# Performance work log

Measured on AMD Instinct MI355X. Metric: run time of the kernel, lower is better.

The kernel has to match this reference:

```python
import jax, jax.numpy as jnp
import numpy as np

B, T, C = 2, 2048, 2048
N_HEAD, N_KV_HEAD = 16, 4
HEAD_DIM = C // N_HEAD  # 128
EPS = 1e-6


def rms_norm(x):
    # no learned scale, normalize over head_dim (last axis)
    return x * jax.lax.rsqrt(jnp.mean(jnp.square(x), axis=-1, keepdims=True) + EPS)


def apply_rotary_emb(x, cos, sin):
    # x: [B, T, H, D]; cos/sin: [T, D/2]  (rotate-half RoPE)
    x1, x2 = jnp.split(x, 2, axis=-1)
    c = cos[None, :, None, :]
    s = sin[None, :, None, :]
    return jnp.concatenate([x1 * c - x2 * s, x1 * s + x2 * c], axis=-1)


def setup_inputs() -> dict:
    key = jax.random.key(0)
    ks = jax.random.split(key, 6)
    x = jax.random.normal(ks[0], (B, T, C), dtype=jnp.float32)
    # real rotary tables: theta = 10000^{-2i/D}
    inv_freq = 1.0 / (10000.0 ** (jnp.arange(0, HEAD_DIM, 2, dtype=jnp.float32) / HEAD_DIM))
    angles = jnp.arange(T, dtype=jnp.float32)[:, None] * inv_freq[None, :]  # [T, D/2]
    cos, sin = jnp.cos(angles), jnp.sin(angles)
    std = 0.02
    Wq = jax.random.normal(ks[1], (C, N_HEAD * HEAD_DIM), dtype=jnp.float32) * std
    Wk = jax.random.normal(ks[2], (C, N_KV_HEAD * HEAD_DIM), dtype=jnp.float32) * std
    Wv = jax.random.normal(ks[3], (C, N_KV_HEAD * HEAD_DIM), dtype=jnp.float32) * std
    Wp = jax.random.normal(ks[4], (C, C), dtype=jnp.float32) * std
    return {"x": x, "cos": cos, "sin": sin, "Wq": Wq, "Wk": Wk, "Wv": Wv, "Wp": Wp}


def reference(x, cos, sin, Wq, Wk, Wv, Wp):
    Bx, Tx, Cx = x.shape
    q = (x @ Wq).reshape(Bx, Tx, N_HEAD, HEAD_DIM)
    k = (x @ Wk).reshape(Bx, Tx, N_KV_HEAD, HEAD_DIM)
    v = (x @ Wv).reshape(Bx, Tx, N_KV_HEAD, HEAD_DIM)
    q = rms_norm(apply_rotary_emb(q, cos, sin))
    k = rms_norm(apply_rotary_emb(k, cos, sin))
    # module scales q by 1/sqrt(D) AND nn.dot_product_attention scales again
    q = q * (1.0 / jnp.sqrt(HEAD_DIM))
    # GQA head repeat
    n_rep = N_HEAD // N_KV_HEAD
    k = jnp.repeat(k, n_rep, axis=2)  # [B, T, H, D]
    v = jnp.repeat(v, n_rep, axis=2)
    scores = jnp.einsum("bthd,bshd->bhts", q, k) / jnp.sqrt(jnp.asarray(HEAD_DIM, x.dtype))
    causal = jnp.tril(jnp.ones((Tx, Tx), dtype=bool))  # key <= query
    scores = jnp.where(causal[None, None, :, :], scores, jnp.finfo(scores.dtype).min)
    probs = jax.nn.softmax(scores, axis=-1)
    y = jnp.einsum("bhts,bshd->bthd", probs, v).reshape(Bx, Tx, Cx)
    return y @ Wp
```

## Files before the change

kernel.cpp:

```cpp
#include <hip/hip_runtime.h>
#include <hip/hip_bf16.h>
#include <math.h>

#define B_  2
#define T_  2048
#define C_  2048
#define NH_ 16
#define NKV_ 4
#define HD_ 128
#define NREP_ (NH_/NKV_)

#define QKVLD 3072
#define KOFF  2048
#define VOFF  2560

#define QSCALE 0.01127105500694502f

typedef __bf16 bf16x8 __attribute__((ext_vector_type(8)));
typedef float  f32x4  __attribute__((ext_vector_type(4)));
typedef float  f32x16 __attribute__((ext_vector_type(16)));

__device__ inline void gload_lds16(const void* g, void* l) {
    __builtin_amdgcn_global_load_lds((const __attribute__((address_space(1))) void*)g,
                                     (__attribute__((address_space(3))) void*)l, 16, 0, 0);
}

__global__ __launch_bounds__(256) void cast_bf16(const float* __restrict__ src,
                                                 __bf16* __restrict__ dst)
{
    size_t i = ((size_t)blockIdx.x * 256 + threadIdx.x) * 8;
    float4 a = *(const float4*)&src[i];
    float4 b = *(const float4*)&src[i + 4];
    union { __bf16 h[8]; uint4 u; } pk;
    pk.h[0] = (__bf16)a.x; pk.h[1] = (__bf16)a.y; pk.h[2] = (__bf16)a.z; pk.h[3] = (__bf16)a.w;
    pk.h[4] = (__bf16)b.x; pk.h[5] = (__bf16)b.y; pk.h[6] = (__bf16)b.z; pk.h[7] = (__bf16)b.w;
    *(uint4*)&dst[i] = pk.u;
}

__global__ __launch_bounds__(256) void wtrans_qkv(const float* __restrict__ Wq,
                                                  const float* __restrict__ Wk,
                                                  const float* __restrict__ Wv,
                                                  __bf16* __restrict__ dst)
{
    __shared__ float tl[32][33];
    int ct = blockIdx.x;
    int k0 = blockIdx.y * 32;
    const float* src;
    int ncols, c0, dr0;
    if (ct < 64)      { src = Wq; ncols = 2048; c0 = ct * 32;        dr0 = ct * 32; }
    else if (ct < 80) { src = Wk; ncols = 512;  c0 = (ct - 64) * 32; dr0 = KOFF + (ct - 64) * 32; }
    else              { src = Wv; ncols = 512;  c0 = (ct - 80) * 32; dr0 = VOFF + (ct - 80) * 32; }

    int tid = threadIdx.x;
    int r  = tid >> 3;
    int c4 = (tid & 7) * 4;
    float4 v = *(const float4*)&src[(size_t)(k0 + r) * ncols + c0 + c4];
    tl[r][c4] = v.x; tl[r][c4 + 1] = v.y; tl[r][c4 + 2] = v.z; tl[r][c4 + 3] = v.w;
    __syncthreads();
    union { __bf16 h[4]; uint2 u; } pk;
#pragma unroll
    for (int j = 0; j < 4; ++j) pk.h[j] = (__bf16)tl[c4 + j][r];
    *(uint2*)&dst[(size_t)(dr0 + r) * 2048 + k0 + c4] = pk.u;
}

__global__ __launch_bounds__(256) void wtrans(const float* __restrict__ src,
                                              __bf16* __restrict__ dst, int ncols)
{
    __shared__ float tl[32][33];
    int n0 = blockIdx.x * 32;
    int k0 = blockIdx.y * 32;
    int tid = threadIdx.x;
    int r  = tid >> 3;
    int c4 = (tid & 7) * 4;
    float4 v = *(const float4*)&src[(size_t)(k0 + r) * ncols + n0 + c4];
    tl[r][c4] = v.x; tl[r][c4 + 1] = v.y; tl[r][c4 + 2] = v.z; tl[r][c4 + 3] = v.w;
    __syncthreads();
    union { __bf16 h[4]; uint2 u; } pk;
#pragma unroll
    for (int j = 0; j < 4; ++j) pk.h[j] = (__bf16)tl[c4 + j][r];
    *(uint2*)&dst[(size_t)(n0 + r) * 2048 + k0 + c4] = pk.u;
}

template<typename TOUT>
__global__ __launch_bounds__(256) void gemm_bt(const __bf16* __restrict__ A,
                                               const __bf16* __restrict__ Bt,
                                               TOUT* __restrict__ C,
                                               int M, int N, int K, int ldc)
{
    __shared__ __bf16 As[2][128 * 32];
    __shared__ __bf16 Bs[2][128 * 32];

    const int tid  = threadIdx.x;
    const int wv   = tid >> 6;
    const int lane = tid & 63;
    const int grp  = lane >> 4;
    const int id16 = lane & 15;
    const int wr   = wv >> 1;
    const int wc   = wv & 1;

    const int row0 = blockIdx.y * 128;
    const int col0 = blockIdx.x * 128;

    const int sm = tid >> 2;
    const int sk = (tid & 3) << 3;

    const __bf16* ga0 = A  + (size_t)(row0 + sm) * K + sk;
    const __bf16* ga1 = A  + (size_t)(row0 + 64 + sm) * K + sk;
    const __bf16* gb0 = Bt + (size_t)(col0 + sm) * K + sk;
    const __bf16* gb1 = Bt + (size_t)(col0 + 64 + sm) * K + sk;

    f32x4 acc[4][4];
    const f32x4 fz = {0.f, 0.f, 0.f, 0.f};
#pragma unroll
    for (int i = 0; i < 4; ++i)
#pragma unroll
        for (int j = 0; j < 4; ++j) acc[i][j] = fz;

    const int nk = K >> 5;

    {
        __bf16* a0 = &As[0][wv << 9];
        __bf16* b0 = &Bs[0][wv << 9];
        gload_lds16(ga0, a0);
        gload_lds16(ga1, a0 + 2048);
        gload_lds16(gb0, b0);
        gload_lds16(gb1, b0 + 2048);
    }

    for (int kt = 0; kt < nk; ++kt) {
        const int bufc = kt & 1;
        asm volatile("s_waitcnt vmcnt(0)" ::: "memory");
        __syncthreads();

        if (kt + 1 < nk) {
            const int kb = (kt + 1) << 5;
            __bf16* a0 = &As[1 - bufc][wv << 9];
            __bf16* b0 = &Bs[1 - bufc][wv << 9];
            gload_lds16(ga0 + kb, a0);
            gload_lds16(ga1 + kb, a0 + 2048);
            gload_lds16(gb0 + kb, b0);
            gload_lds16(gb1 + kb, b0 + 2048);
        }

        bf16x8 af[4], bfr[4];
#pragma unroll
        for (int i = 0; i < 4; ++i)
            af[i] = *(const bf16x8*)&As[bufc][((wr << 6) + (i << 4) + id16) * 32 + (grp << 3)];
#pragma unroll
        for (int j = 0; j < 4; ++j)
            bfr[j] = *(const bf16x8*)&Bs[bufc][((wc << 6) + (j << 4) + id16) * 32 + (grp << 3)];
#pragma unroll
        for (int i = 0; i < 4; ++i)
#pragma unroll
            for (int j = 0; j < 4; ++j)
                acc[i][j] = __builtin_amdgcn_mfma_f32_16x16x32_bf16(af[i], bfr[j], acc[i][j], 0, 0, 0);
    }

#pragma unroll
    for (int i = 0; i < 4; ++i) {
        int gr = row0 + (wr << 6) + (i << 4) + (grp << 2);
#pragma unroll
        for (int j = 0; j < 4; ++j) {
            int gc = col0 + (wc << 6) + (j << 4) + id16;
#pragma unroll
            for (int r = 0; r < 4; ++r) {
                if constexpr (sizeof(TOUT) == 4)
                    C[(size_t)(gr + r) * ldc + gc] = acc[i][j][r];
                else
                    C[(size_t)(gr + r) * ldc + gc] = (TOUT)acc[i][j][r];
            }
        }
    }
}

__global__ __launch_bounds__(256) void rope_rms_b(__bf16* __restrict__ base,
                                                  const float* __restrict__ cosb,
                                                  const float* __restrict__ sinb,
                                                  int nheads, float scale)
{
    int wid  = blockIdx.x * 4 + (threadIdx.x >> 6);
    int lane = threadIdx.x & 63;
    int bt = wid / nheads;
    int hd = wid % nheads;
    int t  = bt % T_;

    __bf16* p = base + (size_t)bt * QKVLD + hd * HD_;
    float c = cosb[t * 64 + lane];
    float s = sinb[t * 64 + lane];
    float x1 = (float)p[lane];
    float x2 = (float)p[lane + 64];
    float r1 = x1 * c - x2 * s;
    float r2 = x1 * s + x2 * c;
    float ss = r1 * r1 + r2 * r2;
#pragma unroll
    for (int off = 32; off; off >>= 1) ss += __shfl_xor(ss, off, 64);
    float inv = rsqrtf(ss * (1.f / 128.f) + 1e-6f) * scale;
    p[lane]      = (__bf16)(r1 * inv);
    p[lane + 64] = (__bf16)(r2 * inv);
}

__global__ __launch_bounds__(256) void vtrans(const __bf16* __restrict__ qkv,
                                              __bf16* __restrict__ vt)
{
    __shared__ __bf16 tl[32][HD_ + 8];
    int bx  = blockIdx.x;
    int st  = bx & 63;
    int bkv = bx >> 6;
    int b = bkv >> 2, kv = bkv & 3;
    int s0 = st << 5;
    int tid = threadIdx.x;
    {
        int s = tid >> 3;
        int d = (tid & 7) << 4;
        const __bf16* src = qkv + (size_t)(b * T_ + s0 + s) * QKVLD + VOFF + kv * HD_ + d;
        *(bf16x8*)&tl[s][d]     = *(const bf16x8*)src;
        *(bf16x8*)&tl[s][d + 8] = *(const bf16x8*)(src + 8);
    }
    __syncthreads();
    {
        int d  = tid >> 1;
        int sh = (tid & 1) << 4;
        __bf16 tmp[16];
#pragma unroll
        for (int j = 0; j < 16; ++j) tmp[j] = tl[sh + j][d];
        __bf16* dst = vt + ((size_t)(b * NKV_ + kv) * HD_ + d) * T_ + s0 + sh;
        *(bf16x8*)dst       = *(bf16x8*)&tmp[0];
        *(bf16x8*)(dst + 8) = *(bf16x8*)&tmp[8];
    }
}

__global__ __launch_bounds__(256, 2) void attn32(const __bf16* __restrict__ qkv,
                                                 const __bf16* __restrict__ vbT,
                                                 __bf16* __restrict__ y,
                                                 float* __restrict__ pOA,
                                                 float* __restrict__ pOB,
                                                 float* __restrict__ pLA,
                                                 float* __restrict__ pLB)
{
    __shared__ __bf16 Ks[2][64 * 128];
    __shared__ __bf16 Vs[2][64 * 128];

    const int tid  = threadIdx.x;
    const int wv   = tid >> 6;
    const int lane = tid & 63;
    const int l31  = lane & 31;
    const int h32  = lane >> 5;

    const int bx   = blockIdx.x;
    const int b    = (bx >> 2) & 1;
    const int kv   = bx & 3;
    const int m    = bx >> 3;
    const int hh   = m & 3;
    const int role = (m >> 2) & 1;
    const int p    = m >> 3;
    const int h    = kv * 4 + hh;
    const int bh   = b * 16 + h;
    const int slot = p * 32 + bh;

    const int hi  = 15 - p;
    const int lo  = p;
    const int tts = role ? (15 - 2 * p) : 99;

    auto KT = [&](int t) { return role ? (t < tts ? 17 + t : t - tts) : t; };

    int qw0 = hi * 128 + wv * 32;
    int qme = qw0 + l31;

    uint koff[4], voff[4];
#pragma unroll
    for (int i = 0; i < 4; ++i) {
        int r  = (wv * 4 + i) * 4 + (lane >> 4);
        int c  = lane & 15;
        int cs = c ^ (r & 15);
        koff[i] = (uint)(r * (QKVLD * 2) + cs * 16);
        int d   = r + ((cs >> 3) << 6);
        voff[i] = (uint)(d * (T_ * 2) + (cs & 7) * 16);
    }
    const char* kg = (const char*)(qkv + (size_t)b * T_ * QKVLD + KOFF + kv * HD_);
    const char* vg = (const char*)(vbT + ((size_t)(b * NKV_ + kv) * HD_) * T_);

    uint off8[8];
#pragma unroll
    for (int s = 0; s < 8; ++s)
        off8[s] = (uint)(l31 * 256 + ((((s << 1) + h32) ^ (l31 & 15)) << 4));

#define STAGE(BUF, KN)                                                        \
    {                                                                         \
        const char* kp = kg + (size_t)(KN) * (64 * QKVLD * 2);                \
        const char* vp = vg + (size_t)(KN) * (64 * 2);                        \
        __bf16* kl = &Ks[BUF][(wv * 4) * 512];                                \
        __bf16* vl = &Vs[BUF][(wv * 4) * 512];                                \
        _Pragma("unroll")                                                     \
        for (int i = 0; i < 4; ++i) gload_lds16(kp + koff[i], kl + i * 512);  \
        _Pragma("unroll")                                                     \
        for (int i = 0; i < 4; ++i) gload_lds16(vp + voff[i], vl + i * 512);  \
    }

    bf16x8 qf[8], qf2[8];
    {
        const __bf16* qp = qkv + (size_t)(b * T_ + hi * 128 + wv * 32 + l31) * QKVLD + h * HD_ + h32 * 8;
#pragma unroll
        for (int s = 0; s < 8; ++s) qf[s] = *(const bf16x8*)(qp + s * 16);
        const __bf16* qp2 = qkv + (size_t)(b * T_ + lo * 128 + wv * 32 + l31) * QKVLD + h * HD_ + h32 * 8;
#pragma unroll
        for (int s = 0; s < 8; ++s) qf2[s] = *(const bf16x8*)(qp2 + s * 16);
    }

    f32x16 o[4];
#pragma unroll
    for (int dt = 0; dt < 4; ++dt)
#pragma unroll
        for (int r = 0; r < 16; ++r) o[dt][r] = 0.f;
    float l_p = 0.f;

#define STORE_PARTIAL(PO, PL)                                                   \
    {                                                                           \
        float lsum = l_p + __shfl_xor(l_p, 32, 64);                             \
        int qloc = wv * 32 + l31;                                               \
        float* po = (PO) + ((size_t)slot * 128 + qloc) * 128;                   \
        _Pragma("unroll")                                                       \
        for (int dt = 0; dt < 4; ++dt)                                          \
            _Pragma("unroll")                                                   \
            for (int g = 0; g < 4; ++g) {                                       \
                float4 f = {o[dt][4 * g + 0], o[dt][4 * g + 1],                 \
                            o[dt][4 * g + 2], o[dt][4 * g + 3]};                \
                *(float4*)&po[dt * 32 + 8 * g + 4 * h32] = f;                   \
            }                                                                   \
        if (h32 == 0) (PL)[slot * 128 + qloc] = lsum;                           \
    }

#define TILE_BODY(TT, BUFC)                                                     \
    {                                                                           \
        const int tt_ = (TT);                                                   \
        asm volatile("s_waitcnt vmcnt(0)" ::: "memory");                        \
        __syncthreads();                                                        \
        if (tt_ + 1 < 17) { int kn_ = KT(tt_ + 1); STAGE(1 - (BUFC), kn_); }    \
        if (role && tt_ == tts) {                                               \
            STORE_PARTIAL(pOB, pLB);                                            \
            _Pragma("unroll")                                                   \
            for (int dt = 0; dt < 4; ++dt)                                      \
                _Pragma("unroll")                                               \
                for (int r = 0; r < 16; ++r) o[dt][r] = 0.f;                    \
            l_p = 0.f;                                                          \
            _Pragma("unroll")                                                   \
            for (int s = 0; s < 8; ++s) qf[s] = qf2[s];                         \
            qw0 = lo * 128 + wv * 32;                                           \
            qme = qw0 + l31;                                                    \
        }                                                                       \
        const int s0 = KT(tt_) << 6;                                            \
        if (s0 <= qw0 + 31) {                                                   \
            const char* Kb = (const char*)&Ks[BUFC][0];                         \
            const char* Vb = (const char*)&Vs[BUFC][0];                         \
            f32x16 S0, S1;                                                      \
            _Pragma("unroll")                                                   \
            for (int r = 0; r < 16; ++r) { S0[r] = 0.f; S1[r] = 0.f; }          \
            __builtin_amdgcn_s_setprio(1);                                      \
            _Pragma("unroll")                                                   \
            for (int s = 0; s < 8; ++s) {                                       \
                bf16x8 kf0 = *(const bf16x8*)(Kb + off8[s]);                    \
                bf16x8 kf1 = *(const bf16x8*)(Kb + off8[s] + 8192);             \
                S0 = __builtin_amdgcn_mfma_f32_32x32x16_bf16(kf0, qf[s], S0, 0, 0, 0); \
                S1 = __builtin_amdgcn_mfma_f32_32x32x16_bf16(kf1, qf[s], S1, 0, 0, 0); \
            }                                                                   \
            __builtin_amdgcn_s_setprio(0);                                      \
            const bool domask = (s0 + 63 > qw0);                                \
            uint w[16];                                                         \
            _Pragma("unroll")                                                   \
            for (int i = 0; i < 8; ++i) {                                       \
                const int r0 = 2 * i;                                           \
                float e0 = exp2f(S0[r0]);                                       \
                float e1 = exp2f(S0[r0 + 1]);                                   \
                if (domask) {                                                   \
                    int k0 = s0 + (r0 & 3) + 8 * (r0 >> 2) + 4 * h32;           \
                    if (k0     > qme) e0 = 0.f;                                 \
                    if (k0 + 1 > qme) e1 = 0.f;                                 \
                }                                                               \
                l_p += e0 + e1;                                                 \
                union { __bf16 h2[2]; uint u; } pk;                             \
                pk.h2[0] = (__bf16)e0; pk.h2[1] = (__bf16)e1;                   \
                w[i] = pk.u;                                                    \
            }                                                                   \
            _Pragma("unroll")                                                   \
            for (int i = 0; i < 8; ++i) {                                       \
                const int r0 = 2 * i;                                           \
                float e0 = exp2f(S1[r0]);                                       \
                float e1 = exp2f(S1[r0 + 1]);                                   \
                if (domask) {                                                   \
                    int k0 = s0 + 32 + (r0 & 3) + 8 * (r0 >> 2) + 4 * h32;      \
                    if (k0     > qme) e0 = 0.f;                                 \
                    if (k0 + 1 > qme) e1 = 0.f;                                 \
                }                                                               \
                l_p += e0 + e1;                                                 \
                union { __bf16 h2[2]; uint u; } pk;                             \
                pk.h2[0] = (__bf16)e0; pk.h2[1] = (__bf16)e1;                   \
                w[8 + i] = pk.u;                                                \
            }                                                                   \
            union U8 { uint u[4]; bf16x8 v; };                                  \
            bf16x8 pf[4];                                                       \
            _Pragma("unroll")                                                   \
            for (int ks = 0; ks < 4; ++ks) {                                    \
                const int bsel = ((ks >> 1) << 3) + ((ks & 1) << 2);            \
                uint sa = h32 ? w[bsel]     : w[bsel + 2];                      \
                uint sb = h32 ? w[bsel + 1] : w[bsel + 3];                      \
                uint g0 = (uint)__shfl_xor((int)sa, 32, 64);                    \
                uint g1 = (uint)__shfl_xor((int)sb, 32, 64);                    \
                U8 t;                                                           \
                if (h32 == 0) {                                                 \
                    t.u[0] = w[bsel];     t.u[1] = w[bsel + 1];                 \
                    t.u[2] = g0;          t.u[3] = g1;                          \
                } else {                                                        \
                    t.u[0] = g0;          t.u[1] = g1;                          \
                    t.u[2] = w[bsel + 2]; t.u[3] = w[bsel + 3];                 \
                }                                                               \
                pf[ks] = t.v;                                                   \
            }                                                                   \
            __builtin_amdgcn_s_setprio(1);                                      \
            _Pragma("unroll")                                                   \
            for (int dt = 0; dt < 4; ++dt) {                                    \
                const int ab = (dt >> 1) << 2;                                  \
                const int hf = (dt & 1) * 8192;                                 \
                _Pragma("unroll")                                               \
                for (int ks = 0; ks < 4; ++ks) {                                \
                    bf16x8 vf = *(const bf16x8*)(Vb + off8[ab + ks] + hf);      \
                    o[dt] = __builtin_amdgcn_mfma_f32_32x32x16_bf16(vf, pf[ks], o[dt], 0, 0, 0); \
                }                                                               \
            }                                                                   \
            __builtin_amdgcn_s_setprio(0);                                      \
        }                                                                       \
    }

    STAGE(0, KT(0));

    for (int tt = 0; tt < 16; tt += 2) {
        TILE_BODY(tt, 0);
        TILE_BODY(tt + 1, 1);
    }
    TILE_BODY(16, 0);

    if (role == 0) {
        STORE_PARTIAL(pOA, pLA);
    } else {
        float l  = l_p + __shfl_xor(l_p, 32, 64);
        float inv = 1.f / l;
        __bf16* yp = y + (size_t)(b * T_ + qw0 + l31) * C_ + h * HD_;
#pragma unroll
        for (int dt = 0; dt < 4; ++dt)
#pragma unroll
            for (int g = 0; g < 4; ++g) {
                union { __bf16 h4[4]; uint2 u; } pk;
#pragma unroll
                for (int e = 0; e < 4; ++e) pk.h4[e] = (__bf16)(o[dt][4 * g + e] * inv);
                *(uint2*)&yp[dt * 32 + 8 * g + 4 * h32] = pk.u;
            }
    }
#undef TILE_BODY
#undef STORE_PARTIAL
#undef STAGE
}

__global__ __launch_bounds__(256) void attn_combine(const float* __restrict__ pOA,
                                                    const float* __restrict__ pOB,
                                                    const float* __restrict__ pLA,
                                                    const float* __restrict__ pLB,
                                                    __bf16* __restrict__ y)
{
    int slot = blockIdx.x;
    int p  = slot >> 5, bh = slot & 31;
    int b  = bh >> 4,   h  = bh & 15;
    int hi = 15 - p;
    int t  = threadIdx.x;
    int q  = t >> 1;
    int dh = (t & 1) << 6;

    float inv = 1.f / (pLA[slot * 128 + q] + pLB[slot * 128 + q]);
    size_t base = ((size_t)slot * 128 + q) * 128 + dh;
    __bf16* yp = y + (size_t)(b * T_ + hi * 128 + q) * C_ + h * HD_ + dh;
#pragma unroll
    for (int d0 = 0; d0 < 64; d0 += 8) {
        float4 a0 = *(const float4*)&pOA[base + d0];
        float4 a1 = *(const float4*)&pOA[base + d0 + 4];
        float4 b0 = *(const float4*)&pOB[base + d0];
        float4 b1 = *(const float4*)&pOB[base + d0 + 4];
        union { __bf16 h8[8]; uint4 u; } pk;
        pk.h8[0] = (__bf16)((a0.x + b0.x) * inv);
        pk.h8[1] = (__bf16)((a0.y + b0.y) * inv);
        pk.h8[2] = (__bf16)((a0.z + b0.z) * inv);
        pk.h8[3] = (__bf16)((a0.w + b0.w) * inv);
        pk.h8[4] = (__bf16)((a1.x + b1.x) * inv);
        pk.h8[5] = (__bf16)((a1.y + b1.y) * inv);
        pk.h8[6] = (__bf16)((a1.z + b1.z) * inv);
        pk.h8[7] = (__bf16)((a1.w + b1.w) * inv);
        *(uint4*)&yp[d0] = pk.u;
    }
}

extern "C" void kernel_launch(void* const* d_in, const int* in_sizes, int n_in,
                              void* d_out, int out_size, void* d_ws, size_t ws_size,
                              hipStream_t stream)
{
    const float* x    = (const float*)d_in[0];
    const float* cosb = (const float*)d_in[1];
    const float* sinb = (const float*)d_in[2];
    const float* Wq   = (const float*)d_in[3];
    const float* Wk   = (const float*)d_in[4];
    const float* Wv   = (const float*)d_in[5];
    const float* Wp   = (const float*)d_in[6];
    float* out = (float*)d_out;

    const int M = B_ * T_;

    char* w = (char*)d_ws;
    __bf16* xb    = (__bf16*)w;  w += (size_t)M * C_ * 2;
    __bf16* qkv   = (__bf16*)w;  w += (size_t)M * QKVLD * 2;
    __bf16* wqkvT = (__bf16*)w;  w += (size_t)QKVLD * C_ * 2;
    __bf16* wpT   = (__bf16*)w;  w += (size_t)C_ * C_ * 2;
    __bf16* vt    = (__bf16*)w;  w += (size_t)M * NKV_ * HD_ * 2;
    __bf16* y     = (__bf16*)w;  w += (size_t)M * C_ * 2;
    float*  pOB   = (float*)w;
    float*  pOA   = (float*)xb;
    float*  pLA   = (float*)wqkvT;
    float*  pLB   = pLA + 8 * 32 * 128;

    cast_bf16<<<(M * C_) / 2048, 256, 0, stream>>>(x, xb);
    wtrans_qkv<<<dim3(96, C_ / 32), 256, 0, stream>>>(Wq, Wk, Wv, wqkvT);
    wtrans<<<dim3(C_ / 32, C_ / 32), 256, 0, stream>>>(Wp, wpT, C_);

    gemm_bt<__bf16><<<dim3(QKVLD / 128, M / 128), 256, 0, stream>>>(xb, wqkvT, qkv, M, QKVLD, C_, QKVLD);

    rope_rms_b<<<(M * NH_) / 4, 256, 0, stream>>>(qkv, cosb, sinb, NH_, QSCALE);
    rope_rms_b<<<(M * NKV_) / 4, 256, 0, stream>>>(qkv + KOFF, cosb, sinb, NKV_, 1.0f);

    vtrans<<<B_ * NKV_ * (T_ / 32), 256, 0, stream>>>(qkv, vt);

    attn32<<<512, 256, 0, stream>>>(qkv, vt, y, pOA, pOB, pLA, pLB);
    attn_combine<<<256, 256, 0, stream>>>(pOA, pOB, pLA, pLB, y);

    gemm_bt<float><<<dim3(C_ / 128, M / 128), 256, 0, stream>>>(y, wpT, out, M, C_, C_, C_);
}
```

Measured before the change: 326.5 us.

## Merge prep and rope/vtrans launches; fold split-attention combine into attention via tickets

Merges the cast and the two weight-transpose kernels into one prep launch, and the Q and K rope/rms passes plus the V transpose into one launch, which also zeroes the per-slot ticket counters. The separate attn_combine kernel is removed. Each split-attention block now writes its partial, fences, and takes an atomic ticket, and the second block to finish reads the other's partial and writes the normalized output. This removes several launches and one full pass over the partial buffers, at the cost of fences, atomics and an extra block barrier inside the attention kernel.

```diff
diff --git a/kernel.cpp b/kernel.cpp
--- a/kernel.cpp
+++ b/kernel.cpp
@@ -25,60 +25,56 @@
                                      (__attribute__((address_space(3))) void*)l, 16, 0, 0);
 }
 
-__global__ __launch_bounds__(256) void cast_bf16(const float* __restrict__ src,
-                                                 __bf16* __restrict__ dst)
-{
-    size_t i = ((size_t)blockIdx.x * 256 + threadIdx.x) * 8;
-    float4 a = *(const float4*)&src[i];
-    float4 b = *(const float4*)&src[i + 4];
-    union { __bf16 h[8]; uint4 u; } pk;
-    pk.h[0] = (__bf16)a.x; pk.h[1] = (__bf16)a.y; pk.h[2] = (__bf16)a.z; pk.h[3] = (__bf16)a.w;
-    pk.h[4] = (__bf16)b.x; pk.h[5] = (__bf16)b.y; pk.h[6] = (__bf16)b.z; pk.h[7] = (__bf16)b.w;
-    *(uint4*)&dst[i] = pk.u;
-}
-
-__global__ __launch_bounds__(256) void wtrans_qkv(const float* __restrict__ Wq,
-                                                  const float* __restrict__ Wk,
-                                                  const float* __restrict__ Wv,
-                                                  __bf16* __restrict__ dst)
+__global__ __launch_bounds__(256) void prep(const float* __restrict__ x,
+                                            const float* __restrict__ Wq,
+                                            const float* __restrict__ Wk,
+                                            const float* __restrict__ Wv,
+                                            const float* __restrict__ Wp,
+                                            __bf16* __restrict__ xb,
+                                            __bf16* __restrict__ wqkvT,
+                                            __bf16* __restrict__ wpT)
 {
     __shared__ float tl[32][33];
-    int ct = blockIdx.x;
-    int k0 = blockIdx.y * 32;
+    const int bx  = blockIdx.x;
+    const int tid = threadIdx.x;
+
+    if (bx < 4096) {
+        size_t i = ((size_t)bx * 256 + tid) * 8;
+        float4 a = *(const float4*)&x[i];
+        float4 b = *(const float4*)&x[i + 4];
+        union { __bf16 h[8]; uint4 u; } pk;
+        pk.h[0] = (__bf16)a.x; pk.h[1] = (__bf16)a.y; pk.h[2] = (__bf16)a.z; pk.h[3] = (__bf16)a.w;
+        pk.h[4] = (__bf16)b.x; pk.h[5] = (__bf16)b.y; pk.h[6] = (__bf16)b.z; pk.h[7] = (__bf16)b.w;
+        *(uint4*)&xb[i] = pk.u;
+        return;
+    }
+
     const float* src;
-    int ncols, c0, dr0;
-    if (ct < 64)      { src = Wq; ncols = 2048; c0 = ct * 32;        dr0 = ct * 32; }
-    else if (ct < 80) { src = Wk; ncols = 512;  c0 = (ct - 64) * 32; dr0 = KOFF + (ct - 64) * 32; }
-    else              { src = Wv; ncols = 512;  c0 = (ct - 80) * 32; dr0 = VOFF + (ct - 80) * 32; }
-
-    int tid = threadIdx.x;
-    int r  = tid >> 3;
+    int ncols, c0, dr0, k0;
+    if (bx < 10240) {
+        int r  = bx - 4096;
+        int ct = r % 96;
+        k0 = (r / 96) * 32;
+        if (ct < 64)      { src = Wq; ncols = 2048; c0 = ct * 32;        dr0 = ct * 32; }
+        else if (ct < 80) { src = Wk; ncols = 512;  c0 = (ct - 64) * 32; dr0 = KOFF + (ct - 64) * 32; }
+        else              { src = Wv; ncols = 512;  c0 = (ct - 80) * 32; dr0 = VOFF + (ct - 80) * 32; }
+    } else {
+        int r  = bx - 10240;
+        src = Wp; ncols = 2048;
+        c0  = (r & 63) * 32; dr0 = c0;
+        k0  = (r >> 6) * 32;
+    }
+    __bf16* dst = (bx < 10240) ? wqkvT : wpT;
+
+    int rr = tid >> 3;
     int c4 = (tid & 7) * 4;
-    float4 v = *(const float4*)&src[(size_t)(k0 + r) * ncols + c0 + c4];
-    tl[r][c4] = v.x; tl[r][c4 + 1] = v.y; tl[r][c4 + 2] = v.z; tl[r][c4 + 3] = v.w;
+    float4 v = *(const float4*)&src[(size_t)(k0 + rr) * ncols + c0 + c4];
+    tl[rr][c4] = v.x; tl[rr][c4 + 1] = v.y; tl[rr][c4 + 2] = v.z; tl[rr][c4 + 3] = v.w;
     __syncthreads();
     union { __bf16 h[4]; uint2 u; } pk;
 #pragma unroll
-    for (int j = 0; j < 4; ++j) pk.h[j] = (__bf16)tl[c4 + j][r];
-    *(uint2*)&dst[(size_t)(dr0 + r) * 2048 + k0 + c4] = pk.u;
-}
-
-__global__ __launch_bounds__(256) void wtrans(const float* __restrict__ src,
-                                              __bf16* __restrict__ dst, int ncols)
-{
-    __shared__ float tl[32][33];
-    int n0 = blockIdx.x * 32;
-    int k0 = blockIdx.y * 32;
-    int tid = threadIdx.x;
-    int r  = tid >> 3;
-    int c4 = (tid & 7) * 4;
-    float4 v = *(const float4*)&src[(size_t)(k0 + r) * ncols + n0 + c4];
-    tl[r][c4] = v.x; tl[r][c4 + 1] = v.y; tl[r][c4 + 2] = v.z; tl[r][c4 + 3] = v.w;
-    __syncthreads();
-    union { __bf16 h[4]; uint2 u; } pk;
-#pragma unroll
-    for (int j = 0; j < 4; ++j) pk.h[j] = (__bf16)tl[c4 + j][r];
-    *(uint2*)&dst[(size_t)(n0 + r) * 2048 + k0 + c4] = pk.u;
+    for (int j = 0; j < 4; ++j) pk.h[j] = (__bf16)tl[c4 + j][rr];
+    *(uint2*)&dst[(size_t)(dr0 + rr) * 2048 + k0 + c4] = pk.u;
 }
 
 template<typename TOUT>
@@ -173,60 +169,66 @@
     }
 }
 
-__global__ __launch_bounds__(256) void rope_rms_b(__bf16* __restrict__ base,
-                                                  const float* __restrict__ cosb,
-                                                  const float* __restrict__ sinb,
-                                                  int nheads, float scale)
-{
-    int wid  = blockIdx.x * 4 + (threadIdx.x >> 6);
-    int lane = threadIdx.x & 63;
-    int bt = wid / nheads;
-    int hd = wid % nheads;
-    int t  = bt % T_;
-
-    __bf16* p = base + (size_t)bt * QKVLD + hd * HD_;
-    float c = cosb[t * 64 + lane];
-    float s = sinb[t * 64 + lane];
-    float x1 = (float)p[lane];
-    float x2 = (float)p[lane + 64];
-    float r1 = x1 * c - x2 * s;
-    float r2 = x1 * s + x2 * c;
-    float ss = r1 * r1 + r2 * r2;
-#pragma unroll
-    for (int off = 32; off; off >>= 1) ss += __shfl_xor(ss, off, 64);
-    float inv = rsqrtf(ss * (1.f / 128.f) + 1e-6f) * scale;
-    p[lane]      = (__bf16)(r1 * inv);
-    p[lane + 64] = (__bf16)(r2 * inv);
-}
-
-__global__ __launch_bounds__(256) void vtrans(const __bf16* __restrict__ qkv,
-                                              __bf16* __restrict__ vt)
+__global__ __launch_bounds__(256) void rope_vt(__bf16* __restrict__ qkv,
+                                               const float* __restrict__ cosb,
+                                               const float* __restrict__ sinb,
+                                               __bf16* __restrict__ vt,
+                                               int* __restrict__ flags)
 {
     __shared__ __bf16 tl[32][HD_ + 8];
-    int bx  = blockIdx.x;
-    int st  = bx & 63;
-    int bkv = bx >> 6;
-    int b = bkv >> 2, kv = bkv & 3;
-    int s0 = st << 5;
-    int tid = threadIdx.x;
-    {
-        int s = tid >> 3;
-        int d = (tid & 7) << 4;
-        const __bf16* src = qkv + (size_t)(b * T_ + s0 + s) * QKVLD + VOFF + kv * HD_ + d;
-        *(bf16x8*)&tl[s][d]     = *(const bf16x8*)src;
-        *(bf16x8*)&tl[s][d + 8] = *(const bf16x8*)(src + 8);
-    }
-    __syncthreads();
-    {
-        int d  = tid >> 1;
-        int sh = (tid & 1) << 4;
-        __bf16 tmp[16];
-#pragma unroll
-        for (int j = 0; j < 16; ++j) tmp[j] = tl[sh + j][d];
-        __bf16* dst = vt + ((size_t)(b * NKV_ + kv) * HD_ + d) * T_ + s0 + sh;
-        *(bf16x8*)dst       = *(bf16x8*)&tmp[0];
-        *(bf16x8*)(dst + 8) = *(bf16x8*)&tmp[8];
-    }
+    const int bx  = blockIdx.x;
+    const int tid = threadIdx.x;
+
+    if (bx < 20480) {
+        int gw   = bx * 4 + (tid >> 6);
+        int lane = tid & 63;
+        int bt = gw / 20;
+        int hd = gw % 20;
+        int t  = bt & (T_ - 1);
+        float scale = (hd < 16) ? QSCALE : 1.0f;
+
+        __bf16* p = qkv + (size_t)bt * QKVLD + hd * HD_;
+        float c = cosb[t * 64 + lane];
+        float s = sinb[t * 64 + lane];
+        float x1 = (float)p[lane];
+        float x2 = (float)p[lane + 64];
+        float r1 = x1 * c - x2 * s;
+        float r2 = x1 * s + x2 * c;
+        float ss = r1 * r1 + r2 * r2;
+#pragma unroll
+        for (int off = 32; off; off >>= 1) ss += __shfl_xor(ss, off, 64);
+        float inv = rsqrtf(ss * (1.f / 128.f) + 1e-6f) * scale;
+        p[lane]      = (__bf16)(r1 * inv);
+        p[lane + 64] = (__bf16)(r2 * inv);
+        return;
+    }
+    if (bx < 20992) {
+        int vbx = bx - 20480;
+        int st  = vbx & 63;
+        int bkv = vbx >> 6;
+        int b = bkv >> 2, kv = bkv & 3;
+        int s0 = st << 5;
+        {
+            int s = tid >> 3;
+            int d = (tid & 7) << 4;
+            const __bf16* src = qkv + (size_t)(b * T_ + s0 + s) * QKVLD + VOFF + kv * HD_ + d;
+            *(bf16x8*)&tl[s][d]     = *(const bf16x8*)src;
+            *(bf16x8*)&tl[s][d + 8] = *(const bf16x8*)(src + 8);
+        }
+        __syncthreads();
+        {
+            int d  = tid >> 1;
+            int sh = (tid & 1) << 4;
+            __bf16 tmp[16];
+#pragma unroll
+            for (int j = 0; j < 16; ++j) tmp[j] = tl[sh + j][d];
+            __bf16* dst = vt + ((size_t)(b * NKV_ + kv) * HD_ + d) * T_ + s0 + sh;
+            *(bf16x8*)dst       = *(bf16x8*)&tmp[0];
+            *(bf16x8*)(dst + 8) = *(bf16x8*)&tmp[8];
+        }
+        return;
+    }
+    flags[tid] = 0;
 }
 
 __global__ __launch_bounds__(256, 2) void attn32(const __bf16* __restrict__ qkv,
@@ -235,10 +237,12 @@
                                                  float* __restrict__ pOA,
                                                  float* __restrict__ pOB,
                                                  float* __restrict__ pLA,
-                                                 float* __restrict__ pLB)
+                                                 float* __restrict__ pLB,
+                                                 int* __restrict__ flags)
 {
     __shared__ __bf16 Ks[2][64 * 128];
     __shared__ __bf16 Vs[2][64 * 128];
+    __shared__ int sh_ticket;
 
     const int tid  = threadIdx.x;
     const int wv   = tid >> 6;
@@ -254,8 +258,7 @@
     const int role = (m >> 2) & 1;
     const int p    = m >> 3;
     const int h    = kv * 4 + hh;
-    const int bh   = b * 16 + h;
-    const int slot = p * 32 + bh;
+    const int slot = p * 32 + b * 16 + h;
 
     const int hi  = 15 - p;
     const int lo  = p;
@@ -313,20 +316,44 @@
         for (int r = 0; r < 16; ++r) o[dt][r] = 0.f;
     float l_p = 0.f;
 
-#define STORE_PARTIAL(PO, PL)                                                   \
+#define FLUSH_COMBINE(POm, PLm, POo, PLo)                                       \
     {                                                                           \
         float lsum = l_p + __shfl_xor(l_p, 32, 64);                             \
         int qloc = wv * 32 + l31;                                               \
-        float* po = (PO) + ((size_t)slot * 128 + qloc) * 128;                   \
+        size_t pbase = ((size_t)slot * 128 + qloc) * 128;                       \
+        float* pom = (POm) + pbase;                                             \
         _Pragma("unroll")                                                       \
         for (int dt = 0; dt < 4; ++dt)                                          \
             _Pragma("unroll")                                                   \
             for (int g = 0; g < 4; ++g) {                                       \
                 float4 f = {o[dt][4 * g + 0], o[dt][4 * g + 1],                 \
                             o[dt][4 * g + 2], o[dt][4 * g + 3]};                \
-                *(float4*)&po[dt * 32 + 8 * g + 4 * h32] = f;                   \
+                *(float4*)&pom[dt * 32 + 8 * g + 4 * h32] = f;                  \
             }                                                                   \
-        if (h32 == 0) (PL)[slot * 128 + qloc] = lsum;                           \
+        if (h32 == 0) (PLm)[slot * 128 + qloc] = lsum;                          \
+        __threadfence();                                                        \
+        __syncthreads();                                                        \
+        if (tid == 0) sh_ticket = atomicAdd(&flags[slot], 1);                   \
+        __syncthreads();                                                        \
+        if (sh_ticket == 1) {                                                   \
+            __threadfence();                                                    \
+            float lo_ = (PLo)[slot * 128 + qloc];                               \
+            float inv = 1.f / (lsum + lo_);                                     \
+            const float* poo = (POo) + pbase;                                   \
+            __bf16* yp = y + (size_t)(b * T_ + hi * 128 + qloc) * C_ + h * HD_; \
+            _Pragma("unroll")                                                   \
+            for (int dt = 0; dt < 4; ++dt)                                      \
+                _Pragma("unroll")                                               \
+                for (int g = 0; g < 4; ++g) {                                   \
+                    float4 f = *(const float4*)&poo[dt * 32 + 8 * g + 4 * h32]; \
+                    union { __bf16 h4[4]; uint2 u; } pk;                        \
+                    pk.h4[0] = (__bf16)((o[dt][4 * g + 0] + f.x) * inv);        \
+                    pk.h4[1] = (__bf16)((o[dt][4 * g + 1] + f.y) * inv);        \
+                    pk.h4[2] = (__bf16)((o[dt][4 * g + 2] + f.z) * inv);        \
+                    pk.h4[3] = (__bf16)((o[dt][4 * g + 3] + f.w) * inv);        \
+                    *(uint2*)&yp[dt * 32 + 8 * g + 4 * h32] = pk.u;             \
+                }                                                               \
+        }                                                                       \
     }
 
 #define TILE_BODY(TT, BUFC)                                                     \
@@ -336,7 +363,7 @@
         __syncthreads();                                                        \
         if (tt_ + 1 < 17) { int kn_ = KT(tt_ + 1); STAGE(1 - (BUFC), kn_); }    \
         if (role && tt_ == tts) {                                               \
-            STORE_PARTIAL(pOB, pLB);                                            \
+            FLUSH_COMBINE(pOB, pLB, pOA, pLA);                                  \
             _Pragma("unroll")                                                   \
             for (int dt = 0; dt < 4; ++dt)                                      \
                 _Pragma("unroll")                                               \
@@ -438,7 +465,7 @@
     TILE_BODY(16, 0);
 
     if (role == 0) {
-        STORE_PARTIAL(pOA, pLA);
+        FLUSH_COMBINE(pOA, pLA, pOB, pLB);
     } else {
         float l  = l_p + __shfl_xor(l_p, 32, 64);
         float inv = 1.f / l;
@@ -454,44 +481,8 @@
             }
     }
 #undef TILE_BODY
-#undef STORE_PARTIAL
+#undef FLUSH_COMBINE
 #undef STAGE
-}
-
-__global__ __launch_bounds__(256) void attn_combine(const float* __restrict__ pOA,
-                                                    const float* __restrict__ pOB,
-                                                    const float* __restrict__ pLA,
-                                                    const float* __restrict__ pLB,
-                                                    __bf16* __restrict__ y)
-{
-    int slot = blockIdx.x;
-    int p  = slot >> 5, bh = slot & 31;
-    int b  = bh >> 4,   h  = bh & 15;
-    int hi = 15 - p;
-    int t  = threadIdx.x;
-    int q  = t >> 1;
-    int dh = (t & 1) << 6;
-
-    float inv = 1.f / (pLA[slot * 128 + q] + pLB[slot * 128 + q]);
-    size_t base = ((size_t)slot * 128 + q) * 128 + dh;
-    __bf16* yp = y + (size_t)(b * T_ + hi * 128 + q) * C_ + h * HD_ + dh;
-#pragma unroll
-    for (int d0 = 0; d0 < 64; d0 += 8) {
-        float4 a0 = *(const float4*)&pOA[base + d0];
-        float4 a1 = *(const float4*)&pOA[base + d0 + 4];
-        float4 b0 = *(const float4*)&pOB[base + d0];
-        float4 b1 = *(const float4*)&pOB[base + d0 + 4];
-        union { __bf16 h8[8]; uint4 u; } pk;
-        pk.h8[0] = (__bf16)((a0.x + b0.x) * inv);
-        pk.h8[1] = (__bf16)((a0.y + b0.y) * inv);
-        pk.h8[2] = (__bf16)((a0.z + b0.z) * inv);
-        pk.h8[3] = (__bf16)((a0.w + b0.w) * inv);
-        pk.h8[4] = (__bf16)((a1.x + b1.x) * inv);
-        pk.h8[5] = (__bf16)((a1.y + b1.y) * inv);
-        pk.h8[6] = (__bf16)((a1.z + b1.z) * inv);
-        pk.h8[7] = (__bf16)((a1.w + b1.w) * inv);
-        *(uint4*)&yp[d0] = pk.u;
-    }
 }
 
 extern "C" void kernel_launch(void* const* d_in, const int* in_sizes, int n_in,
@@ -516,24 +507,19 @@
     __bf16* wpT   = (__bf16*)w;  w += (size_t)C_ * C_ * 2;
     __bf16* vt    = (__bf16*)w;  w += (size_t)M * NKV_ * HD_ * 2;
     __bf16* y     = (__bf16*)w;  w += (size_t)M * C_ * 2;
-    float*  pOB   = (float*)w;
+    float*  pOB   = (float*)w;   w += (size_t)8 * 32 * 128 * 128 * 4;
+    int*    flags = (int*)w;
     float*  pOA   = (float*)xb;
     float*  pLA   = (float*)wqkvT;
     float*  pLB   = pLA + 8 * 32 * 128;
 
-    cast_bf16<<<(M * C_) / 2048, 256, 0, stream>>>(x, xb);
-    wtrans_qkv<<<dim3(96, C_ / 32), 256, 0, stream>>>(Wq, Wk, Wv, wqkvT);
-    wtrans<<<dim3(C_ / 32, C_ / 32), 256, 0, stream>>>(Wp, wpT, C_);
+    prep<<<14336, 256, 0, stream>>>(x, Wq, Wk, Wv, Wp, xb, wqkvT, wpT);
 
     gemm_bt<__bf16><<<dim3(QKVLD / 128, M / 128), 256, 0, stream>>>(xb, wqkvT, qkv, M, QKVLD, C_, QKVLD);
 
-    rope_rms_b<<<(M * NH_) / 4, 256, 0, stream>>>(qkv, cosb, sinb, NH_, QSCALE);
-    rope_rms_b<<<(M * NKV_) / 4, 256, 0, stream>>>(qkv + KOFF, cosb, sinb, NKV_, 1.0f);
-
-    vtrans<<<B_ * NKV_ * (T_ / 32), 256, 0, stream>>>(qkv, vt);
-
-    attn32<<<512, 256, 0, stream>>>(qkv, vt, y, pOA, pOB, pLA, pLB);
-    attn_combine<<<256, 256, 0, stream>>>(pOA, pOB, pLA, pLB, y);
+    rope_vt<<<20993, 256, 0, stream>>>(qkv, cosb, sinb, vt, flags);
+
+    attn32<<<512, 256, 0, stream>>>(qkv, vt, y, pOA, pOB, pLA, pLB, flags);
 
     gemm_bt<float><<<dim3(C_ / 128, M / 128), 256, 0, stream>>>(y, wpT, out, M, C_, C_, C_);
 }
```

New measurement: 403.2 us. 1.23x slower.
